# Performance work log

Hardware: AMD Instinct MI355X
Metric: run time of the kernel (lower is better)

Reference implementation:

```python
import jax, jax.numpy as jnp
import numpy as np
from jax import lax

B, V, C, H, W = 2, 8, 64, 128, 128
A = 256
C3 = 3 * C + 2  # 194 input channels for refine/confidence branches
CO = 3 * C      # 192 output channels of branch_refine
GROUPS = 8      # _group_count(192, 8) == 8
HID = max(4, CO // 4)  # 48 hidden channels in ChannelGate2d


def _conv3(x, w, b):
    y = lax.conv_general_dilated(x, w, (1, 1), 'SAME',
                                 dimension_numbers=('NCHW', 'OIHW', 'NCHW'))
    return y + b[None, :, None, None]


def _group_norm(x, scale, bias, groups, eps=1e-5):
    b, c, h, w = x.shape
    xg = x.reshape(b, groups, c // groups, h, w)
    mu = xg.mean(axis=(2, 3, 4), keepdims=True)
    var = xg.var(axis=(2, 3, 4), keepdims=True)
    xn = ((xg - mu) / jnp.sqrt(var + eps)).reshape(b, c, h, w)
    return xn * scale[None, :, None, None] + bias[None, :, None, None]


def _channel_gate(x, w1, b1, w2, b2):
    pooled = x.mean(axis=(2, 3))                     # [B,C]
    h = jax.nn.silu(pooled @ w1.T + b1)              # [B,HID]
    gate = jax.nn.sigmoid(h @ w2.T + b2)             # [B,C]
    return x * (0.5 + gate)[:, :, None, None]


def _conv_block(x, p):
    h = jax.nn.silu(_group_norm(_conv3(x, p['c1w'], p['c1b']), p['g1s'], p['g1b'], GROUPS))
    h = jax.nn.silu(_group_norm(_conv3(h, p['c2w'], p['c2b']), p['g2s'], p['g2b'], GROUPS))
    h = _channel_gate(h, p['gw1'], p['gb1'], p['gw2'], p['gb2'])
    res = jnp.einsum('bchw,oc->bohw', x, p['rpw']) + p['rpb'][None, :, None, None]
    return h + jnp.tanh(p['rs']) * res


def _fuse(vf, uvs, masks, importance, atlas_size):
    # vf:[B,V,C,H,W] uvs:[B,V,H,W,2] masks:[B,V,1,H,W] importance:[B,V]
    b, v, c, h, w = vf.shape
    P = atlas_size * atlas_size
    weights = jnp.maximum(importance.astype(vf.dtype), 0.0)
    finite = jnp.isfinite(uvs).all(axis=-1)                 # [B,V,H,W]
    valid = (masks[:, :, 0] > 0.5) & finite & (weights[:, :, None, None] > 0.0)
    safe = jnp.where(finite[..., None], uvs, 0.0)
    xi = jnp.round(jnp.clip(safe[..., 0], 0.0, 1.0) * (atlas_size - 1)).astype(jnp.int32)
    yi = jnp.round((1.0 - jnp.clip(safe[..., 1], 0.0, 1.0)) * (atlas_size - 1)).astype(jnp.int32)
    idx = (yi * atlas_size + xi).reshape(b, v * h * w)      # [B,N]
    wvalid = valid.astype(vf.dtype) * weights[:, :, None, None]
    feat = (vf * wvalid[:, :, None]).transpose(0, 2, 1, 3, 4).reshape(b, c, v * h * w)
    cnt = wvalid.reshape(b, v * h * w)

    def per_sample(f, cc, i):
        atlas = jax.ops.segment_sum(f.T, i, num_segments=P).T   # [C,P]
        counts = jax.ops.segment_sum(cc, i, num_segments=P)     # [P]
        return atlas, counts

    atlas, counts = jax.vmap(per_sample)(feat, cnt, idx)
    atlas = atlas.reshape(b, c, atlas_size, atlas_size)
    counts = counts.reshape(b, 1, atlas_size, atlas_size)
    fused = atlas / jnp.maximum(counts, 1.0)
    return fused, (counts > 0).astype(vf.dtype)


def _normalize_per_sample(t, eps=1e-6):
    scale = jnp.maximum(t.reshape(t.shape[0], -1).max(axis=1), eps)
    return jnp.clip(t / scale[:, None, None, None], 0.0, 1.0)


def setup_inputs() -> dict:
    key = jax.random.key(0)
    ks = jax.random.split(key, 20)
    inp = {
        'encoded_views': jax.random.normal(ks[0], (B, V, C, H, W), jnp.float32),
        'view_uvs': jax.random.uniform(ks[1], (B, V, H, W, 2), jnp.float32),
        'view_masks': jax.random.uniform(ks[2], (B, V, 1, H, W), jnp.float32),
        'w_global': jax.random.uniform(ks[3], (B, V), jnp.float32),
        'w_boundary': jax.random.uniform(ks[4], (B, V), jnp.float32),
        'w_highlight': jax.random.uniform(ks[5], (B, V), jnp.float32),
        'atlas_size': A,
        # ConvBlock params (random instead of zero-init so all paths are exercised)
        'c1w': jax.random.normal(ks[6], (CO, C3, 3, 3), jnp.float32) * 0.02,
        'c1b': jnp.zeros((CO,), jnp.float32),
        'g1s': jnp.ones((CO,), jnp.float32),
        'g1b': jnp.zeros((CO,), jnp.float32),
        'c2w': jax.random.normal(ks[7], (CO, CO, 3, 3), jnp.float32) * 0.02,
        'c2b': jnp.zeros((CO,), jnp.float32),
        'g2s': jnp.ones((CO,), jnp.float32),
        'g2b': jnp.zeros((CO,), jnp.float32),
        'gw1': jax.random.normal(ks[8], (HID, CO), jnp.float32) * 0.05,
        'gb1': jnp.zeros((HID,), jnp.float32),
        'gw2': jax.random.normal(ks[9], (CO, HID), jnp.float32) * 0.05,
        'gb2': jnp.zeros((CO,), jnp.float32),
        'rpw': jax.random.normal(ks[10], (CO, C3), jnp.float32) * 0.05,
        'rpb': jnp.zeros((CO,), jnp.float32),
        'rs': jnp.array(0.3, jnp.float32),
        'conf_w': jax.random.normal(ks[11], (3, C3), jnp.float32) * 0.05,
        'conf_b': jnp.zeros((3,), jnp.float32),
        'mix_scale': jnp.array(0.5, jnp.float32),
    }
    return inp


def reference(encoded_views, view_uvs, view_masks, w_global, w_boundary, w_highlight,
              atlas_size, c1w, c1b, g1s, g1b, c2w, c2b, g2s, g2b,
              gw1, gb1, gw2, gb2, rpw, rpb, rs, conf_w, conf_b, mix_scale):
    p = dict(c1w=c1w, c1b=c1b, g1s=g1s, g1b=g1b, c2w=c2w, c2b=c2b, g2s=g2s, g2b=g2b,
             gw1=gw1, gb1=gb1, gw2=gw2, gb2=gb2, rpw=rpw, rpb=rpb, rs=rs)
    g_feat, g_val = _fuse(encoded_views, view_uvs, view_masks, w_global, atlas_size)
    b_feat, b_val = _fuse(encoded_views, view_uvs, view_masks, w_boundary, atlas_size)
    h_feat, h_val = _fuse(encoded_views, view_uvs, view_masks, w_highlight, atlas_size)
    coverage = jnp.clip((g_val + b_val + h_val) / 3.0, 0.0, 1.0)
    stack = jnp.stack([g_feat, b_feat, h_feat], axis=1)     # [B,3,C,A,A]
    uncertainty = jnp.sqrt(stack.var(axis=1).mean(axis=1, keepdims=True))
    uncertainty = _normalize_per_sample(uncertainty) * coverage
    ctx = jnp.concatenate([g_feat, b_feat, h_feat, coverage, uncertainty], axis=1)
    refine = _conv_block(ctx, p)
    rg, rb, rh = jnp.split(refine, 3, axis=1)
    conf = jax.nn.sigmoid(jnp.einsum('bchw,oc->bohw', ctx, conf_w) + conf_b[None, :, None, None])
    ms = jnp.tanh(mix_scale)
    g_out = g_feat + ms * rg * conf[:, 0:1]
    b_out = b_feat + ms * rb * conf[:, 1:2]
    h_out = h_feat + ms * rh * conf[:, 2:3]
    return (g_out, b_out, h_out, coverage, uncertainty, conf)
```

## Files before the change

kernel.cpp:

```cpp
#include <hip/hip_runtime.h>
#include <math.h>

#define B_ 2
#define V_ 8
#define C_ 64
#define HW_ 16384
#define A_ 256
#define P_ 65536
#define CO_ 192
#define CPG_ 24
#define NG_ 8
#define ICP1 224
#define ICP2 192

#define OFF_ACC   0ull
#define SZ_ACC    (2ull*65536*192*4)
#define OFF_CNT   (OFF_ACC + SZ_ACC)
#define SZ_CNT    (2ull*3*65536*4)
#define OFF_CTXB  (OFF_CNT + SZ_CNT)
#define SZ_CTXB   (2ull*65536*224*2)
#define OFF_H1A   (OFF_CTXB + SZ_CTXB)
#define SZ_H1A    (2ull*65536*192*2)
#define OFF_W1    (OFF_H1A + SZ_H1A)
#define SZ_W1     (9ull*192*224*2)
#define OFF_W2    (OFF_W1 + SZ_W1)
#define SZ_W2     (9ull*192*192*2)
#define OFF_SM    (OFF_W2 + SZ_W2 + 256)

#define SM_STATS1 0
#define SM_STATS2 256
#define SM_SCALE  512
#define SM_POOLED 1024
#define SM_GATE   2560
#define SM_RAWU   8192
#define SM_CONFP  532480

#define OUT_B    8388608
#define OUT_COV  25165824
#define OUT_UNC  25296896
#define OUT_CONF 25427968

typedef __attribute__((ext_vector_type(4))) float f32x4;
typedef __attribute__((ext_vector_type(8))) short bf16x8;

__device__ __forceinline__ float sigmoidf_(float x){ return 1.f/(1.f+expf(-x)); }
__device__ __forceinline__ float bf2f(unsigned short h){ return __uint_as_float(((unsigned)h)<<16); }
__device__ __forceinline__ unsigned short f2bf(float f){
  unsigned u = __float_as_uint(f);
  return (unsigned short)((u + 0x7fffu + ((u>>16)&1u)) >> 16);
}

__device__ __forceinline__ void gl_lds16(const void* g, void* l){
  __builtin_amdgcn_global_load_lds((const __attribute__((address_space(1))) void*)g,
                                   (__attribute__((address_space(3))) void*)l, 16, 0, 0);
}

__global__ __launch_bounds__(256) void k_prep(const float* __restrict__ c1w,
    const float* __restrict__ c2w, unsigned short* __restrict__ w1p, unsigned short* __restrict__ w2p)
{
  int idx = blockIdx.x*256 + threadIdx.x;
  const int N1 = 9*192*224;
  if (idx < N1){
    int ic = idx % 224; int oc = (idx/224) % 192; int k = idx/(224*192);
    float v = (ic < 194) ? c1w[(size_t)(oc*194+ic)*9 + k] : 0.f;
    w1p[idx] = f2bf(v);
  } else {
    int i2 = idx - N1;
    if (i2 < 9*192*192){
      int ic = i2 % 192; int oc = (i2/192) % 192; int k = i2/(192*192);
      w2p[i2] = f2bf(c2w[(size_t)(oc*192+ic)*9 + k]);
    }
  }
}

__global__ __launch_bounds__(256) void k_fuse(const float* __restrict__ vf,
    const float* __restrict__ uvs, const float* __restrict__ masks,
    const float* __restrict__ wgp, const float* __restrict__ wbp, const float* __restrict__ whp,
    float* __restrict__ acc, float* __restrict__ cnt)
{
  __shared__ __align__(16) float sf[64*65];
  __shared__ int sidx[64];
  __shared__ int svalid[64];
  __shared__ float sw[3];
  int t = threadIdx.x;
  int pix0 = blockIdx.x*64;
  int b   = pix0 / (V_*HW_);
  int rem = pix0 % (V_*HW_);
  int v   = rem / HW_;
  int p2  = rem % HW_;
  size_t vbase = ((size_t)(b*V_+v))*C_*HW_;
  for (int i=0;i<4;i++){
    int f = t + i*256;
    int c = f>>4, px4 = (f&15)*4;
    float4 vv = *(const float4*)&vf[vbase + (size_t)c*HW_ + p2 + px4];
    float* d = &sf[c*65+px4];
    d[0]=vv.x; d[1]=vv.y; d[2]=vv.z; d[3]=vv.w;
  }
  if (t<64){
    const float* u2 = uvs + (((size_t)(b*V_+v))*HW_ + p2 + t)*2;
    float ux = u2[0], uy = u2[1];
    int fin = isfinite(ux) && isfinite(uy);
    float su = fin?ux:0.f, svv = fin?uy:0.f;
    float cu = fminf(fmaxf(su,0.f),1.f);
    float cv = fminf(fmaxf(svv,0.f),1.f);
    int xi = (int)rintf(cu*255.f);
    int yi = (int)rintf((1.f-cv)*255.f);
    sidx[t] = yi*256+xi;
    float m = masks[((size_t)(b*V_+v))*HW_ + p2 + t];
    svalid[t] = (m>0.5f) && fin;
  }
  if (t<3){
    const float* wp = (t==0)?wgp:((t==1)?wbp:whp);
    sw[t] = fmaxf(wp[b*V_+v], 0.f);
  }
  __syncthreads();
  int wave = t>>6, lane = t&63;
  float w0 = sw[0], w1 = sw[1], w2 = sw[2];
  for (int i=0;i<16;i++){
    int px = wave*16+i;
    if (!svalid[px]) continue;
    int bin = sidx[px];
    float val = sf[lane*65+px];
    size_t base = ((size_t)b*P_ + bin)*192;
    if (w0>0.f) atomicAdd(&acc[base + lane],        val*w0);
    if (w1>0.f) atomicAdd(&acc[base + 64 + lane],   val*w1);
    if (w2>0.f) atomicAdd(&acc[base + 128 + lane],  val*w2);
    if (lane<3){
      float wv = sw[lane];
      if (wv>0.f) atomicAdd(&cnt[((size_t)(b*3+lane))*P_ + bin], wv);
    }
  }
}

__global__ __launch_bounds__(256) void k_finalize(const float* __restrict__ acc,
      const float* __restrict__ cnt, unsigned short* __restrict__ ctxb,
      float* __restrict__ out_cov, float* __restrict__ raw_unc, int* __restrict__ scale,
      const float* __restrict__ cw, const float* __restrict__ cbias, float* __restrict__ confp)
{
  __shared__ __align__(16) float sv[64*193];
  __shared__ float sc[3][64];
  __shared__ float up[256];
  __shared__ float up3[3][256];
  __shared__ float s_cov[64];
  __shared__ float s_unc[64];
  __shared__ float scw[582];
  int t = threadIdx.x;
  int bin0 = blockIdx.x*64;
  int b = bin0 >> 16;
  int p0 = bin0 & 65535;
  size_t abase = ((size_t)b*P_ + p0)*192;
  for (int f=t; f<582; f+=256) scw[f] = cw[f];
  for (int i=0;i<48;i++){
    int f = t + i*256;
    int bl = f/192, c = f - bl*192;
    sv[bl*193+c] = acc[abase + f];
  }
  if (t<192){
    int br = t>>6, bl = t&63;
    sc[br][bl] = cnt[((size_t)(b*3+br))*P_ + p0 + bl];
  }
  __syncthreads();
  {
    int bl = t>>2, q = t&3;
    float dg = 1.f/fmaxf(sc[0][bl],1.f);
    float db = 1.f/fmaxf(sc[1][bl],1.f);
    float dh = 1.f/fmaxf(sc[2][bl],1.f);
    float s = 0.f;
    for (int j=0;j<16;j++){
      int c = q*16+j;
      float fg = sv[bl*193+c]*dg;
      float fb = sv[bl*193+64+c]*db;
      float fh = sv[bl*193+128+c]*dh;
      sv[bl*193+c]=fg; sv[bl*193+64+c]=fb; sv[bl*193+128+c]=fh;
      float m = (fg+fb+fh)*(1.f/3.f);
      float d0=fg-m, d1=fb-m, d2=fh-m;
      s += d0*d0+d1*d1+d2*d2;
    }
    up[t] = s;
  }
  __syncthreads();
  if (t<64){
    float tot = up[t*4]+up[t*4+1]+up[t*4+2]+up[t*4+3];
    float u = sqrtf(tot*(1.f/192.f));
    float vg = sc[0][t]>0.f?1.f:0.f;
    float vb = sc[1][t]>0.f?1.f:0.f;
    float vh = sc[2][t]>0.f?1.f:0.f;
    float cov = fminf(fmaxf((vg+vb+vh)*(1.f/3.f),0.f),1.f);
    s_cov[t] = cov; s_unc[t] = u;
    out_cov[(size_t)b*P_ + p0 + t] = cov;
    raw_unc[(size_t)b*P_ + p0 + t] = u;
    atomicMax(&scale[b], __float_as_int(u));
  }
  __syncthreads();
  {
    int bl = t>>2, q = t&3;
    float q0=0.f,q1=0.f,q2=0.f;
    for (int j=0;j<16;j++){
      int c = q*16+j;
      float fg = sv[bl*193+c];
      float fb = sv[bl*193+64+c];
      float fh = sv[bl*193+128+c];
      q0 += fg*scw[c]     + fb*scw[64+c]     + fh*scw[128+c];
      q1 += fg*scw[194+c] + fb*scw[258+c]    + fh*scw[322+c];
      q2 += fg*scw[388+c] + fb*scw[452+c]    + fh*scw[516+c];
    }
    up3[0][t]=q0; up3[1][t]=q1; up3[2][t]=q2;
  }
  __syncthreads();
  if (t<64){
    float cov = s_cov[t];
    #pragma unroll
    for (int o=0;o<3;o++){
      float pdot = up3[o][t*4]+up3[o][t*4+1]+up3[o][t*4+2]+up3[o][t*4+3]
                 + cov*scw[o*194+192] + cbias[o];
      confp[((size_t)(b*3+o))*P_ + p0 + t] = pdot;
    }
  }
  for (int f=t; f<1792; f+=256){
    int cg = f % 28, bl = f / 28;
    int c0 = cg*8;
    unsigned short h[8];
    #pragma unroll
    for (int j=0;j<8;j++){
      int c = c0+j;
      float vv;
      if (c < 192)      vv = sv[bl*193+c];
      else if (c==192)  vv = s_cov[bl];
      else if (c==193)  vv = s_unc[bl];
      else              vv = 0.f;
      h[j] = f2bf(vv);
    }
    *(uint4*)&ctxb[((size_t)b*P_ + p0 + bl)*ICP1 + c0] = *(uint4*)h;
  }
}

__global__ __launch_bounds__(256) void k_norm_unc(unsigned short* __restrict__ ctxb,
    const int* __restrict__ scale, const float* __restrict__ raw_unc,
    const float* __restrict__ out_cov, float* __restrict__ out_unc,
    const float* __restrict__ confp, const float* __restrict__ cw, float* __restrict__ out_conf)
{
  int tid = blockIdx.x*256 + threadIdx.x;
  int b = tid >> 16, p = tid & 65535;
  float s = fmaxf(__int_as_float(scale[b]), 1e-6f);
  float u = raw_unc[tid];
  float cov = out_cov[tid];
  float un = fminf(fmaxf(u/s,0.f),1.f)*cov;
  out_unc[tid] = un;
  ctxb[(size_t)tid*ICP1 + 193] = f2bf(un);
  float w0 = cw[193], w1 = cw[387], w2 = cw[581];
  out_conf[((size_t)(b*3+0))*P_ + p] = sigmoidf_(confp[((size_t)(b*3+0))*P_ + p] + w0*un);
  out_conf[((size_t)(b*3+1))*P_ + p] = sigmoidf_(confp[((size_t)(b*3+1))*P_ + p] + w1*un);
  out_conf[((size_t)(b*3+2))*P_ + p] = sigmoidf_(confp[((size_t)(b*3+2))*P_ + p] + w2*un);
}

template<int ICP, int CHUNKS>
__global__ __launch_bounds__(256,2) void k_conv3(const unsigned short* __restrict__ X,
    const unsigned short* __restrict__ Wp, const float* __restrict__ bias, unsigned short* __restrict__ Y,
    double* __restrict__ stats)
{
  __shared__ short s_in[2][258*32];
  __shared__ short s_w[576*32];
  __shared__ float sred[2][64];
  __shared__ float gsm[16];
  int t = threadIdx.x;
  int f_ = blockIdx.x + 128*(blockIdx.y + 3*blockIdx.z);
  int xcd = f_ & 7; int g_ = f_ >> 3;
  int ypair = xcd*16 + (g_ & 15);
  int h_  = g_ >> 4;
  int b   = h_ & 1;
  int oc0 = (h_ >> 1)*64;
  int y0  = ypair*2;
  int wv = t>>6, lane = t&63, l15 = lane&15, quad = lane>>4;

  f32x4 accA[4][4], accB[4][4];
  #pragma unroll
  for (int mt=0;mt<4;mt++){
    float4 bv = *(const float4*)&bias[oc0 + mt*16 + quad*4];
    f32x4 iv; iv.x=bv.x; iv.y=bv.y; iv.z=bv.z; iv.w=bv.w;
    #pragma unroll
    for (int nt=0;nt<4;nt++){ accA[mt][nt]=iv; accB[mt][nt]=iv; }
  }

  const unsigned short* Xb = X + (size_t)b*P_*ICP;

  if (t < 128){
    int bufi = t>>6, j = t&63;
    int idx = (j<32) ? j : (257*32 + (j-32));
    s_in[bufi][idx] = 0;
  }
  if (t < 128) sred[t>>6][t&63] = 0.f;
  if (t < 16)  gsm[t] = 0.f;

  auto issue_input = [&](int c2, int j2){
    int gy = y0 - 1 + j2;
    gy = min(max(gy,0),255);
    const unsigned short* src = Xb + ((size_t)gy*256)*ICP + c2*32;
    short* dst = &s_in[j2&1][0];
    #pragma unroll
    for (int i=0;i<4;i++){
      int f = t + i*256;
      int xi = 1 + (f>>2), icq = f&3;
      int icg = icq ^ ((xi>>1)&3);
      gl_lds16(src + (size_t)(xi-1)*ICP + icg*8, dst + 32 + (size_t)f*8);
    }
  };
  auto issue_wa = [&](int c2){
    int ic0n = c2*32;
    #pragma unroll
    for (int i=0;i<6;i++){
      int f = t + i*256;
      int oc = (f>>2)&63, icq = f&3;
      int r = i*64 + oc;
      int icg = icq ^ ((r>>1)&3);
      gl_lds16(Wp + ((size_t)(i*192) + oc0 + oc)*ICP + ic0n + icg*8, &s_w[(size_t)f*8]);
    }
  };
  auto issue_wb = [&](int c2){
    int ic0n = c2*32;
    #pragma unroll
    for (int i=0;i<3;i++){
      int f = t + i*256;
      int oc = (f>>2)&63, icq = f&3;
      int r = (6+i)*64 + oc;
      int icg = icq ^ ((r>>1)&3);
      gl_lds16(Wp + ((size_t)((6+i)*192) + oc0 + oc)*ICP + ic0n + icg*8, &s_w[(size_t)(1536+f)*8]);
    }
  };

  issue_wa(0);
  issue_input(0,0);
  issue_wb(0);
  issue_input(0,1);
  asm volatile("s_waitcnt lgkmcnt(0)" ::: "memory");

  for (int c=0; c<CHUNKS; ++c){
    #pragma unroll
    for (int j=0;j<4;++j){
      if (j==0)      asm volatile("s_waitcnt vmcnt(7)" ::: "memory");
      else if (j==1) asm volatile("s_waitcnt vmcnt(4)" ::: "memory");
      else if (j==2) asm volatile("s_waitcnt vmcnt(4)" ::: "memory");
      else {
        if (c==CHUNKS-1) asm volatile("s_waitcnt vmcnt(0)"  ::: "memory");
        else             asm volatile("s_waitcnt vmcnt(10)" ::: "memory");
      }
      __builtin_amdgcn_s_barrier();
      __builtin_amdgcn_sched_barrier(0);

      bool doA = (j<=2) && (y0 + j >= 1);
      bool doB = (j>=1) && (y0 - 1 + j <= 255);
      const short* si = &s_in[j&1][0];
      if (doA || doB){
        #pragma unroll
        for (int kx=0;kx<3;kx++){
          bf16x8 Bf[4];
          #pragma unroll
          for (int nt=0;nt<4;nt++){
            int r = wv*64 + nt*16 + l15 + kx;
            Bf[nt] = *(const bf16x8*)&si[r*32 + ((quad ^ ((r>>1)&3)))*8];
          }
          if (doA){
            bf16x8 Af[4];
            #pragma unroll
            for (int mt=0;mt<4;mt++){
              int r = j*192 + kx*64 + mt*16 + l15;
              Af[mt] = *(const bf16x8*)&s_w[r*32 + ((quad ^ ((r>>1)&3)))*8];
            }
            #pragma unroll
            for (int mt=0;mt<4;mt++)
              #pragma unroll
              for (int nt=0;nt<4;nt++)
                accA[mt][nt] = __builtin_amdgcn_mfma_f32_16x16x32_bf16(Af[mt], Bf[nt], accA[mt][nt], 0, 0, 0);
          }
          if (doB){
            bf16x8 Af[4];
            #pragma unroll
            for (int mt=0;mt<4;mt++){
              int r = (j-1)*192 + kx*64 + mt*16 + l15;
              Af[mt] = *(const bf16x8*)&s_w[r*32 + ((quad ^ ((r>>1)&3)))*8];
            }
            #pragma unroll
            for (int mt=0;mt<4;mt++)
              #pragma unroll
              for (int nt=0;nt<4;nt++)
                accB[mt][nt] = __builtin_amdgcn_mfma_f32_16x16x32_bf16(Af[mt], Bf[nt], accB[mt][nt], 0, 0, 0);
          }
        }
      }
      __builtin_amdgcn_s_barrier();
      __builtin_amdgcn_sched_barrier(0);
      if (j==2 && c+1<CHUNKS) issue_wa(c+1);
      if (j==3 && c+1<CHUNKS) issue_wb(c+1);
      if (!(c==CHUNKS-1 && j>=2))
        issue_input(j>=2 ? c+1 : c, (j+2)&3);
    }
  }

  unsigned short* Yb = Y + (size_t)b*P_*192;
  #pragma unroll
  for (int mt=0;mt<4;mt++){
    int oc = oc0 + mt*16 + quad*4;
    #pragma unroll
    for (int nt=0;nt<4;nt++){
      int px = wv*64 + nt*16 + l15;
      f32x4 a = accA[mt][nt];
      ushort4 ha; ha.x=f2bf(a.x); ha.y=f2bf(a.y); ha.z=f2bf(a.z); ha.w=f2bf(a.w);
      *(ushort4*)&Yb[(size_t)(y0*256+px)*192 + oc] = ha;
      f32x4 bb = accB[mt][nt];
      ushort4 hb; hb.x=f2bf(bb.x); hb.y=f2bf(bb.y); hb.z=f2bf(bb.z); hb.w=f2bf(bb.w);
      *(ushort4*)&Yb[(size_t)((y0+1)*256+px)*192 + oc] = hb;
    }
  }

  #pragma unroll
  for (int mt=0;mt<4;mt++)
    #pragma unroll
    for (int jj=0;jj<4;jj++){
      float v1 = accA[mt][0][jj]+accA[mt][1][jj]+accA[mt][2][jj]+accA[mt][3][jj]
               + accB[mt][0][jj]+accB[mt][1][jj]+accB[mt][2][jj]+accB[mt][3][jj];
      float v2 = accA[mt][0][jj]*accA[mt][0][jj]+accA[mt][1][jj]*accA[mt][1][jj]
               + accA[mt][2][jj]*accA[mt][2][jj]+accA[mt][3][jj]*accA[mt][3][jj]
               + accB[mt][0][jj]*accB[mt][0][jj]+accB[mt][1][jj]*accB[mt][1][jj]
               + accB[mt][2][jj]*accB[mt][2][jj]+accB[mt][3][jj]*accB[mt][3][jj];
      v1 += __shfl_xor(v1,1); v1 += __shfl_xor(v1,2); v1 += __shfl_xor(v1,4); v1 += __shfl_xor(v1,8);
      v2 += __shfl_xor(v2,1); v2 += __shfl_xor(v2,2); v2 += __shfl_xor(v2,4); v2 += __shfl_xor(v2,8);
      if (l15==0){
        int ocl = mt*16 + quad*4 + jj;
        atomicAdd(&sred[0][ocl], v1);
        atomicAdd(&sred[1][ocl], v2);
      }
    }
  __syncthreads();
  if (t < 64){
    int g = (oc0 + t)/24;
    atomicAdd(&gsm[g*2],   sred[0][t]);
    atomicAdd(&gsm[g*2+1], sred[1][t]);
  }
  __syncthreads();
  if (t < 8){
    int glo = oc0/24, ghi = (oc0+63)/24;
    if (t >= glo && t <= ghi){
      atomicAdd(&stats[(b*8+t)*2],   (double)gsm[t*2]);
      atomicAdd(&stats[(b*8+t)*2+1], (double)gsm[t*2+1]);
    }
  }
}

__global__ __launch_bounds__(256) void k_gn1_apply(const unsigned short* __restrict__ x, const double* __restrict__ stats,
    const float* __restrict__ gs, const float* __restrict__ gb, unsigned short* __restrict__ y)
{
  size_t i8 = ((size_t)blockIdx.x*256 + threadIdx.x)*8;
  int b = (int)(i8 / ((size_t)192*P_));
  int c = (int)(i8 % 192);
  int bg = b*8 + c/24;
  const double N = 24.0*65536.0;
  double mu = stats[bg*2]/N;
  double var = stats[bg*2+1]/N - mu*mu;
  float rstd = 1.0f/sqrtf((float)var + 1e-5f);
  float mean = (float)mu;
  float4 sA = *(const float4*)&gs[c];
  float4 sB = *(const float4*)&gs[c+4];
  float4 bA = *(const float4*)&gb[c];
  float4 bB = *(const float4*)&gb[c+4];
  uint4 vv = *(const uint4*)&x[i8];
  unsigned wd[4] = {vv.x,vv.y,vv.z,vv.w};
  float scl[8] = {sA.x,sA.y,sA.z,sA.w,sB.x,sB.y,sB.z,sB.w};
  float bia[8] = {bA.x,bA.y,bA.z,bA.w,bB.x,bB.y,bB.z,bB.w};
  unsigned short h[8];
  #pragma unroll
  for (int i=0;i<8;i++){
    unsigned bits = wd[i>>1];
    float xi = (i&1) ? __uint_as_float(bits & 0xffff0000u) : __uint_as_float(bits<<16);
    float xn = (xi-mean)*rstd*scl[i] + bia[i];
    h[i] = f2bf(xn*sigmoidf_(xn));
  }
  *(uint4*)&y[i8] = *(uint4*)h;
}

__global__ __launch_bounds__(256) void k_gn2_apply(unsigned short* __restrict__ x, const double* __restrict__ stats,
    const float* __restrict__ gs, const float* __restrict__ gb, float* __restrict__ pooled)
{
  __shared__ float pl[384];
  int t = threadIdx.x;
  for (int f=t; f<384; f+=256) pl[f]=0.f;
  int tid = blockIdx.x*256 + t;
  int c = (tid*8) % 192;
  float4 sA = *(const float4*)&gs[c];
  float4 sB = *(const float4*)&gs[c+4];
  float4 bA = *(const float4*)&gb[c];
  float4 bB = *(const float4*)&gb[c+4];
  float scl[8] = {sA.x,sA.y,sA.z,sA.w,sB.x,sB.y,sB.z,sB.w};
  float bia[8] = {bA.x,bA.y,bA.z,bA.w,bB.x,bB.y,bB.z,bB.w};
  float mean[2], rstd[2];
  #pragma unroll
  for (int bb=0;bb<2;bb++){
    int bg = bb*8 + c/24;
    const double N = 24.0*65536.0;
    double mu = stats[bg*2]/N;
    double var = stats[bg*2+1]/N - mu*mu;
    rstd[bb] = 1.0f/sqrtf((float)var + 1e-5f);
    mean[bb] = (float)mu;
  }
  float pacc[2][8] = {{0.f}};
  __syncthreads();
  #pragma unroll
  for (int k=0;k<8;k++){
    size_t i8 = ((size_t)tid + (size_t)k*393216)*8;
    int bb = k>>2;
    uint4 vv = *(const uint4*)&x[i8];
    unsigned wd[4] = {vv.x,vv.y,vv.z,vv.w};
    unsigned short h[8];
    #pragma unroll
    for (int i=0;i<8;i++){
      unsigned bits = wd[i>>1];
      float xi = (i&1) ? __uint_as_float(bits & 0xffff0000u) : __uint_as_float(bits<<16);
      float xn = (xi-mean[bb])*rstd[bb]*scl[i] + bia[i];
      xn = xn*sigmoidf_(xn);
      h[i] = f2bf(xn);
      pacc[bb][i] += bf2f(h[i]);
    }
    *(uint4*)&x[i8] = *(uint4*)h;
  }
  #pragma unroll
  for (int bb=0;bb<2;bb++)
    #pragma unroll
    for (int i=0;i<8;i++) atomicAdd(&pl[bb*192 + c + i], pacc[bb][i]);
  __syncthreads();
  for (int f=t; f<384; f+=256) atomicAdd(&pooled[f], pl[f]*(1.f/65536.f));
}

__global__ void k_gate(const float* __restrict__ pooled, const float* __restrict__ gw1,
    const float* __restrict__ gb1, const float* __restrict__ gw2, const float* __restrict__ gb2,
    float* __restrict__ gatef)
{
  __shared__ float hb[2*48];
  int t = threadIdx.x;
  if (t<96){
    int b=t/48, j=t%48;
    float a = gb1[j];
    for (int c=0;c<192;c++) a = fmaf(pooled[b*192+c], gw1[j*192+c], a);
    hb[t] = a*sigmoidf_(a);
  }
  __syncthreads();
  for (int i=t;i<384;i+=256){
    int b=i/192, c=i%192;
    float a = gb2[c];
    for (int j=0;j<48;j++) a = fmaf(hb[b*48+j], gw2[c*48+j], a);
    gatef[i] = 0.5f + sigmoidf_(a);
  }
}

__global__ __launch_bounds__(256,4) void k_combine(const unsigned short* __restrict__ ctxb,
    const unsigned short* __restrict__ h2, const float* __restrict__ rpw, const float* __restrict__ rpb,
    const float* __restrict__ gatef, const float* __restrict__ conf_out,
    const float* __restrict__ rs, const float* __restrict__ mix, float* __restrict__ dout)
{
  __shared__ short s_x[256*32];
  __shared__ short s_w[64*32];
  int t = threadIdx.x;
  size_t p0 = (size_t)blockIdx.x*256;
  int oc0 = blockIdx.y*64, br = blockIdx.y;
  int wv = t>>6, lane = t&63, l15 = lane&15, quad = lane>>4;
  f32x4 acc[4][4];
  #pragma unroll
  for (int mt=0;mt<4;mt++){
    float4 bv = *(const float4*)&rpb[oc0 + mt*16 + quad*4];
    f32x4 iv; iv.x=bv.x; iv.y=bv.y; iv.z=bv.z; iv.w=bv.w;
    #pragma unroll
    for (int nt=0;nt<4;nt++) acc[mt][nt]=iv;
  }
  for (int ch=0; ch<7; ch++){
    int ic0 = ch*32;
    __syncthreads();
    for (int f=t; f<1024; f+=256){
      int icq = f&3, px = f>>2;
      uint4 v = *(const uint4*)&ctxb[(p0+px)*ICP1 + ic0 + icq*8];
      *(uint4*)&s_x[px*32 + ((icq ^ ((px>>1)&3)))*8] = v;
    }
    {
      int oc = t&63, icq = t>>6;
      unsigned short h[8];
      #pragma unroll
      for (int j=0;j<8;j++){
        int ic = ic0 + icq*8 + j;
        h[j] = (ic<194) ? f2bf(rpw[(size_t)(oc0+oc)*194 + ic]) : (unsigned short)0;
      }
      *(uint4*)&s_w[oc*32 + ((icq ^ ((oc>>1)&3)))*8] = *(uint4*)h;
    }
    __syncthreads();
    bf16x8 Af[4], Bf[4];
    #pragma unroll
    for (int mt=0;mt<4;mt++){
      int r = mt*16 + l15;
      Af[mt] = *(const bf16x8*)&s_w[r*32 + (((quad ^ ((r>>1)&3)))&3)*8];
    }
    #pragma unroll
    for (int nt=0;nt<4;nt++){
      int r = wv*64 + nt*16 + l15;
      Bf[nt] = *(const bf16x8*)&s_x[r*32 + (((quad ^ ((r>>1)&3)))&3)*8];
    }
    #pragma unroll
    for (int mt=0;mt<4;mt++)
      #pragma unroll
      for (int nt=0;nt<4;nt++)
        acc[mt][nt] = __builtin_amdgcn_mfma_f32_16x16x32_bf16(Af[mt], Bf[nt], acc[mt][nt], 0, 0, 0);
  }
  float trs = tanhf(rs[0]);
  float ms2 = tanhf(mix[0]);
  int b = (int)(p0 >> 16);
  #pragma unroll
  for (int mt=0;mt<4;mt++){
    int oc = oc0 + mt*16 + quad*4;
    int cc = oc & 63;
    float4 gv = *(const float4*)&gatef[b*192 + oc];
    #pragma unroll
    for (int nt=0;nt<4;nt++){
      size_t pf = p0 + wv*64 + nt*16 + l15;
      int p = (int)(pf & 65535);
      ushort4 fh = *(const ushort4*)&ctxb[pf*ICP1 + oc];
      ushort4 hh = *(const ushort4*)&h2[pf*192 + oc];
      float cf = conf_out[((size_t)(b*3+br))*P_ + p];
      size_t dst = (size_t)br*OUT_B + ((size_t)(b*64+cc))*P_ + p;
      dout[dst]            = bf2f(fh.x) + ms2*(bf2f(hh.x)*gv.x + trs*acc[mt][nt].x)*cf;
      dout[dst + P_]       = bf2f(fh.y) + ms2*(bf2f(hh.y)*gv.y + trs*acc[mt][nt].y)*cf;
      dout[dst + 2*P_]     = bf2f(fh.z) + ms2*(bf2f(hh.z)*gv.z + trs*acc[mt][nt].z)*cf;
      dout[dst + 3*P_]     = bf2f(fh.w) + ms2*(bf2f(hh.w)*gv.w + trs*acc[mt][nt].w)*cf;
    }
  }
}

extern "C" void kernel_launch(void* const* d_in, const int* in_sizes, int n_in,
                              void* d_out, int out_size, void* d_ws, size_t ws_size,
                              hipStream_t stream)
{
  const float* vf    = (const float*)d_in[0];
  const float* uvs   = (const float*)d_in[1];
  const float* masks = (const float*)d_in[2];
  const float* wg    = (const float*)d_in[3];
  const float* wb    = (const float*)d_in[4];
  const float* wh    = (const float*)d_in[5];
  const float* c1w = (const float*)d_in[7];
  const float* c1b = (const float*)d_in[8];
  const float* g1s = (const float*)d_in[9];
  const float* g1b = (const float*)d_in[10];
  const float* c2w = (const float*)d_in[11];
  const float* c2b = (const float*)d_in[12];
  const float* g2s = (const float*)d_in[13];
  const float* g2b = (const float*)d_in[14];
  const float* gw1 = (const float*)d_in[15];
  const float* gb1 = (const float*)d_in[16];
  const float* gw2 = (const float*)d_in[17];
  const float* gb2 = (const float*)d_in[18];
  const float* rpw = (const float*)d_in[19];
  const float* rpb = (const float*)d_in[20];
  const float* rs  = (const float*)d_in[21];
  const float* cw  = (const float*)d_in[22];
  const float* cb  = (const float*)d_in[23];
  const float* mix = (const float*)d_in[24];

  char* ws = (char*)d_ws;
  float*          accb  = (float*)(ws + OFF_ACC);
  float*          cntb  = (float*)(ws + OFF_CNT);
  unsigned short* ctxb  = (unsigned short*)(ws + OFF_CTXB);
  unsigned short* h1act = (unsigned short*)(ws + OFF_H1A);
  unsigned short* w1p   = (unsigned short*)(ws + OFF_W1);
  unsigned short* w2p   = (unsigned short*)(ws + OFF_W2);
  unsigned short* h1pre = (unsigned short*)(ws + OFF_ACC);
  unsigned short* h2    = (unsigned short*)(ws + OFF_ACC);
  double* stats1 = (double*)(ws + OFF_SM + SM_STATS1);
  double* stats2 = (double*)(ws + OFF_SM + SM_STATS2);
  int*    scale  = (int*)(ws + OFF_SM + SM_SCALE);
  float*  pooled = (float*)(ws + OFF_SM + SM_POOLED);
  float*  gatef  = (float*)(ws + OFF_SM + SM_GATE);
  float*  rawu   = (float*)(ws + OFF_SM + SM_RAWU);
  float*  confp  = (float*)(ws + OFF_SM + SM_CONFP);

  float* out = (float*)d_out;
  float* out_cov  = out + OUT_COV;
  float* out_unc  = out + OUT_UNC;
  float* out_conf = out + OUT_CONF;

  hipMemsetAsync(ws + OFF_ACC, 0, SZ_ACC + SZ_CNT, stream);
  hipMemsetAsync(ws + OFF_SM, 0, 8192, stream);

  k_prep<<<2808, 256, 0, stream>>>(c1w, c2w, w1p, w2p);
  k_fuse<<<4096, 256, 0, stream>>>(vf, uvs, masks, wg, wb, wh, accb, cntb);
  k_finalize<<<2048, 256, 0, stream>>>(accb, cntb, ctxb, out_cov, rawu, scale, cw, cb, confp);
  k_norm_unc<<<512, 256, 0, stream>>>(ctxb, scale, rawu, out_cov, out_unc, confp, cw, out_conf);
  k_conv3<ICP1,7><<<dim3(128,3,2), 256, 0, stream>>>(ctxb, w1p, c1b, h1pre, stats1);
  k_gn1_apply<<<12288, 256, 0, stream>>>(h1pre, stats1, g1s, g1b, h1act);
  k_conv3<ICP2,6><<<dim3(128,3,2), 256, 0, stream>>>(h1act, w2p, c2b, h2, stats2);
  k_gn2_apply<<<1536, 256, 0, stream>>>(h2, stats2, g2s, g2b, pooled);
  k_gate<<<1, 256, 0, stream>>>(pooled, gw1, gb1, gw2, gb2, gatef);
  k_combine<<<dim3(512,3), 256, 0, stream>>>(ctxb, h2, rpw, rpb, gatef, out_conf, rs, mix, out);
}
```

Before: 718.4 us.

## Split conv3 into 8 waves with dedicated input and weight loader roles

Doubles the conv3 block to 512 threads. Each wave now computes a single output row instead of two, so the accumulator set is halved. Waves 0-3 issue the input-row loads while waves 4-7 issue the weight loads, each group with its own vmcnt waits, and MFMA sections are wrapped in s_setprio to favour math over loads. The aim is more waves to hide load latency and lower register pressure per wave. The raised __launch_bounds__(512,4) may squeeze registers enough to cause spills, and LDS use likely still caps occupancy.

```diff
diff --git a/kernel.cpp b/kernel.cpp
--- a/kernel.cpp
+++ b/kernel.cpp
@@ -254,7 +254,7 @@
 }
 
 template<int ICP, int CHUNKS>
-__global__ __launch_bounds__(256,2) void k_conv3(const unsigned short* __restrict__ X,
+__global__ __launch_bounds__(512,4) void k_conv3(const unsigned short* __restrict__ X,
     const unsigned short* __restrict__ Wp, const float* __restrict__ bias, unsigned short* __restrict__ Y,
     double* __restrict__ stats)
 {
@@ -270,15 +270,18 @@
   int b   = h_ & 1;
   int oc0 = (h_ >> 1)*64;
   int y0  = ypair*2;
-  int wv = t>>6, lane = t&63, l15 = lane&15, quad = lane>>4;
-
-  f32x4 accA[4][4], accB[4][4];
+  int w = t>>6, lane = t&63, l15 = lane&15, quad = lane>>4;
+  int pxw = (w&3);
+  int rw  = (w>>2);
+  bool inputRole = (w < 4);
+
+  f32x4 acc[4][4];
   #pragma unroll
   for (int mt=0;mt<4;mt++){
     float4 bv = *(const float4*)&bias[oc0 + mt*16 + quad*4];
     f32x4 iv; iv.x=bv.x; iv.y=bv.y; iv.z=bv.z; iv.w=bv.w;
     #pragma unroll
-    for (int nt=0;nt<4;nt++){ accA[mt][nt]=iv; accB[mt][nt]=iv; }
+    for (int nt=0;nt<4;nt++) acc[mt][nt]=iv;
   }
 
   const unsigned short* Xb = X + (size_t)b*P_*ICP;
@@ -306,108 +309,104 @@
   };
   auto issue_wa = [&](int c2){
     int ic0n = c2*32;
+    int t2 = t - 256;
     #pragma unroll
     for (int i=0;i<6;i++){
-      int f = t + i*256;
+      int f = t2 + i*256;
       int oc = (f>>2)&63, icq = f&3;
-      int r = i*64 + oc;
+      int r = (f>>8)*64 + oc;
       int icg = icq ^ ((r>>1)&3);
-      gl_lds16(Wp + ((size_t)(i*192) + oc0 + oc)*ICP + ic0n + icg*8, &s_w[(size_t)f*8]);
+      gl_lds16(Wp + ((size_t)((f>>8)*192) + oc0 + oc)*ICP + ic0n + icg*8, &s_w[(size_t)f*8]);
     }
   };
   auto issue_wb = [&](int c2){
     int ic0n = c2*32;
+    int t2 = t - 256;
     #pragma unroll
     for (int i=0;i<3;i++){
-      int f = t + i*256;
+      int f = t2 + i*256;
       int oc = (f>>2)&63, icq = f&3;
-      int r = (6+i)*64 + oc;
+      int r = (6+(f>>8))*64 + oc;
       int icg = icq ^ ((r>>1)&3);
-      gl_lds16(Wp + ((size_t)((6+i)*192) + oc0 + oc)*ICP + ic0n + icg*8, &s_w[(size_t)(1536+f)*8]);
+      gl_lds16(Wp + ((size_t)((6+(f>>8))*192) + oc0 + oc)*ICP + ic0n + icg*8, &s_w[(size_t)(1536+f)*8]);
     }
   };
 
-  issue_wa(0);
-  issue_input(0,0);
-  issue_wb(0);
-  issue_input(0,1);
+  if (inputRole){
+    issue_input(0,0);
+    issue_input(0,1);
+  } else {
+    issue_wa(0);
+    issue_wb(0);
+  }
   asm volatile("s_waitcnt lgkmcnt(0)" ::: "memory");
 
   for (int c=0; c<CHUNKS; ++c){
     #pragma unroll
     for (int j=0;j<4;++j){
-      if (j==0)      asm volatile("s_waitcnt vmcnt(7)" ::: "memory");
-      else if (j==1) asm volatile("s_waitcnt vmcnt(4)" ::: "memory");
-      else if (j==2) asm volatile("s_waitcnt vmcnt(4)" ::: "memory");
-      else {
-        if (c==CHUNKS-1) asm volatile("s_waitcnt vmcnt(0)"  ::: "memory");
-        else             asm volatile("s_waitcnt vmcnt(10)" ::: "memory");
+      if (c==CHUNKS-1 && j==3){
+        asm volatile("s_waitcnt vmcnt(0)" ::: "memory");
+      } else if (inputRole){
+        asm volatile("s_waitcnt vmcnt(4)" ::: "memory");
+      } else {
+        if (j==0 || j==1)      asm volatile("s_waitcnt vmcnt(3)" ::: "memory");
+        else if (j==2)         asm volatile("s_waitcnt vmcnt(0)" ::: "memory");
       }
       __builtin_amdgcn_s_barrier();
       __builtin_amdgcn_sched_barrier(0);
 
       bool doA = (j<=2) && (y0 + j >= 1);
       bool doB = (j>=1) && (y0 - 1 + j <= 255);
+      bool mine = rw ? doB : doA;
+      int kyr = rw ? (j-1) : j;
       const short* si = &s_in[j&1][0];
-      if (doA || doB){
+      if (mine){
+        __builtin_amdgcn_s_setprio(1);
         #pragma unroll
         for (int kx=0;kx<3;kx++){
           bf16x8 Bf[4];
           #pragma unroll
           for (int nt=0;nt<4;nt++){
-            int r = wv*64 + nt*16 + l15 + kx;
+            int r = pxw*64 + nt*16 + l15 + kx;
             Bf[nt] = *(const bf16x8*)&si[r*32 + ((quad ^ ((r>>1)&3)))*8];
           }
-          if (doA){
-            bf16x8 Af[4];
+          bf16x8 Af[4];
+          #pragma unroll
+          for (int mt=0;mt<4;mt++){
+            int r = kyr*192 + kx*64 + mt*16 + l15;
+            Af[mt] = *(const bf16x8*)&s_w[r*32 + ((quad ^ ((r>>1)&3)))*8];
+          }
+          #pragma unroll
+          for (int mt=0;mt<4;mt++)
             #pragma unroll
-            for (int mt=0;mt<4;mt++){
-              int r = j*192 + kx*64 + mt*16 + l15;
-              Af[mt] = *(const bf16x8*)&s_w[r*32 + ((quad ^ ((r>>1)&3)))*8];
-            }
-            #pragma unroll
-            for (int mt=0;mt<4;mt++)
-              #pragma unroll
-              for (int nt=0;nt<4;nt++)
-                accA[mt][nt] = __builtin_amdgcn_mfma_f32_16x16x32_bf16(Af[mt], Bf[nt], accA[mt][nt], 0, 0, 0);
-          }
-          if (doB){
-            bf16x8 Af[4];
-            #pragma unroll
-            for (int mt=0;mt<4;mt++){
-              int r = (j-1)*192 + kx*64 + mt*16 + l15;
-              Af[mt] = *(const bf16x8*)&s_w[r*32 + ((quad ^ ((r>>1)&3)))*8];
-            }
-            #pragma unroll
-            for (int mt=0;mt<4;mt++)
-              #pragma unroll
-              for (int nt=0;nt<4;nt++)
-                accB[mt][nt] = __builtin_amdgcn_mfma_f32_16x16x32_bf16(Af[mt], Bf[nt], accB[mt][nt], 0, 0, 0);
-          }
+            for (int nt=0;nt<4;nt++)
+              acc[mt][nt] = __builtin_amdgcn_mfma_f32_16x16x32_bf16(Af[mt], Bf[nt], acc[mt][nt], 0, 0, 0);
         }
+        __builtin_amdgcn_s_setprio(0);
       }
       __builtin_amdgcn_s_barrier();
       __builtin_amdgcn_sched_barrier(0);
-      if (j==2 && c+1<CHUNKS) issue_wa(c+1);
-      if (j==3 && c+1<CHUNKS) issue_wb(c+1);
-      if (!(c==CHUNKS-1 && j>=2))
-        issue_input(j>=2 ? c+1 : c, (j+2)&3);
+      if (inputRole){
+        if (!(c==CHUNKS-1 && j>=2))
+          issue_input(j>=2 ? c+1 : c, (j+2)&3);
+      } else {
+        if (j==2 && c+1<CHUNKS) issue_wa(c+1);
+        if (j==3 && c+1<CHUNKS) issue_wb(c+1);
+      }
     }
   }
 
   unsigned short* Yb = Y + (size_t)b*P_*192;
+  int yrow = y0 + rw;
   #pragma unroll
   for (int mt=0;mt<4;mt++){
     int oc = oc0 + mt*16 + quad*4;
     #pragma unroll
     for (int nt=0;nt<4;nt++){
-      int px = wv*64 + nt*16 + l15;
-      f32x4 a = accA[mt][nt];
+      int px = pxw*64 + nt*16 + l15;
+      f32x4 a = acc[mt][nt];
       ushort4 ha; ha.x=f2bf(a.x); ha.y=f2bf(a.y); ha.z=f2bf(a.z); ha.w=f2bf(a.w);
-      *(ushort4*)&Yb[(size_t)(y0*256+px)*192 + oc] = ha;
-      f32x4 bb = accB[mt][nt];
-      ushort4 hb; hb.x=f2bf(bb.x); hb.y=f2bf(bb.y); hb.z=f2bf(bb.z); hb.w=f2bf(bb.w);
-      *(ushort4*)&Yb[(size_t)((y0+1)*256+px)*192 + oc] = hb;
+      *(ushort4*)&Yb[(size_t)(yrow*256+px)*192 + oc] = ha;
     }
   }
 
@@ -415,12 +414,9 @@
   for (int mt=0;mt<4;mt++)
     #pragma unroll
     for (int jj=0;jj<4;jj++){
-      float v1 = accA[mt][0][jj]+accA[mt][1][jj]+accA[mt][2][jj]+accA[mt][3][jj]
-               + accB[mt][0][jj]+accB[mt][1][jj]+accB[mt][2][jj]+accB[mt][3][jj];
-      float v2 = accA[mt][0][jj]*accA[mt][0][jj]+accA[mt][1][jj]*accA[mt][1][jj]
-               + accA[mt][2][jj]*accA[mt][2][jj]+accA[mt][3][jj]*accA[mt][3][jj]
-               + accB[mt][0][jj]*accB[mt][0][jj]+accB[mt][1][jj]*accB[mt][1][jj]
-               + accB[mt][2][jj]*accB[mt][2][jj]+accB[mt][3][jj]*accB[mt][3][jj];
+      float v1 = acc[mt][0][jj]+acc[mt][1][jj]+acc[mt][2][jj]+acc[mt][3][jj];
+      float v2 = acc[mt][0][jj]*acc[mt][0][jj]+acc[mt][1][jj]*acc[mt][1][jj]
+               + acc[mt][2][jj]*acc[mt][2][jj]+acc[mt][3][jj]*acc[mt][3][jj];
       v1 += __shfl_xor(v1,1); v1 += __shfl_xor(v1,2); v1 += __shfl_xor(v1,4); v1 += __shfl_xor(v1,8);
       v2 += __shfl_xor(v2,1); v2 += __shfl_xor(v2,2); v2 += __shfl_xor(v2,4); v2 += __shfl_xor(v2,8);
       if (l15==0){
@@ -686,9 +682,9 @@
   k_fuse<<<4096, 256, 0, stream>>>(vf, uvs, masks, wg, wb, wh, accb, cntb);
   k_finalize<<<2048, 256, 0, stream>>>(accb, cntb, ctxb, out_cov, rawu, scale, cw, cb, confp);
   k_norm_unc<<<512, 256, 0, stream>>>(ctxb, scale, rawu, out_cov, out_unc, confp, cw, out_conf);
-  k_conv3<ICP1,7><<<dim3(128,3,2), 256, 0, stream>>>(ctxb, w1p, c1b, h1pre, stats1);
+  k_conv3<ICP1,7><<<dim3(128,3,2), 512, 0, stream>>>(ctxb, w1p, c1b, h1pre, stats1);
   k_gn1_apply<<<12288, 256, 0, stream>>>(h1pre, stats1, g1s, g1b, h1act);
-  k_conv3<ICP2,6><<<dim3(128,3,2), 256, 0, stream>>>(h1act, w2p, c2b, h2, stats2);
+  k_conv3<ICP2,6><<<dim3(128,3,2), 512, 0, stream>>>(h1act, w2p, c2b, h2, stats2);
   k_gn2_apply<<<1536, 256, 0, stream>>>(h2, stats2, g2s, g2b, pooled);
   k_gate<<<1, 256, 0, stream>>>(pooled, gw1, gb1, gw2, gb2, gatef);
   k_combine<<<dim3(512,3), 256, 0, stream>>>(ctxb, h2, rpw, rpb, gatef, out_conf, rs, mix, out);
```

After: 967.4 us. +34.7%, slower.
